# Performance work log

Measured on AMD Instinct MI355X. Metric: run time of the kernel, lower is better.

## Reference

```python
import jax, jax.numpy as jnp
import numpy as np

N_NODES = 100000
N_EDGES = 1600000
IN_FEATS = 64
N_CLASSES = 64


def setup_inputs() -> dict:
    key = jax.random.key(0)
    k1, k2, k3, k4, k5 = jax.random.split(key, 5)
    feat = jax.random.normal(k1, (N_NODES, IN_FEATS), dtype=jnp.float32)
    edge_row = jnp.sort(jax.random.randint(k2, (N_EDGES,), 0, N_NODES))
    edge_col = jax.random.randint(k3, (N_EDGES,), 0, N_NODES)
    # values of the cached normalized adjacency power (all positive, ~1/deg scale)
    edge_val = jax.random.uniform(k4, (N_EDGES,), dtype=jnp.float32) / 16.0
    # nn.Linear(in_feats, n_classes): weight [C, F] (xavier), bias zeros
    limit = float(np.sqrt(6.0 / (IN_FEATS + N_CLASSES)))
    W = jax.random.uniform(k5, (N_CLASSES, IN_FEATS), dtype=jnp.float32,
                           minval=-limit, maxval=limit)
    b = jnp.zeros((N_CLASSES,), dtype=jnp.float32)
    return {"feat": feat, "edge_row": edge_row, "edge_col": edge_col,
            "edge_val": edge_val, "W": W, "b": b}


def reference(feat, edge_row, edge_col, edge_val, W, b):
    # SpMM: h = A_pre @ feat, A_pre given as COO (edge_row, edge_col, edge_val)
    msg = edge_val[:, None] * feat[edge_col]          # [E, F] gather + scale
    h = jax.ops.segment_sum(msg, edge_row, num_segments=N_NODES)  # [N, F]
    # fc: Linear(in_feats -> n_classes), norm=None so no normalization
    return h @ W.T + b                                 # [N, C]
```

## Files before the change

kernel.cpp:

```cpp
#include <hip/hip_runtime.h>
#include <hip/hip_bf16.h>

typedef __attribute__((ext_vector_type(8))) short short8;
typedef __attribute__((ext_vector_type(4))) float f32x4;

__device__ __forceinline__ unsigned short f2bf(float x) {
    unsigned int u = __float_as_uint(x);
    unsigned int lsb = (u >> 16) & 1u;
    u += 0x7fffu + lsb;
    return (unsigned short)(u >> 16);
}

__device__ __forceinline__ float bf2f(unsigned short b) {
    return __uint_as_float(((unsigned int)b) << 16);
}

__device__ __forceinline__ short8 pack8(float4 a, float4 b) {
    short8 r;
    r[0] = (short)f2bf(a.x); r[1] = (short)f2bf(a.y);
    r[2] = (short)f2bf(a.z); r[3] = (short)f2bf(a.w);
    r[4] = (short)f2bf(b.x); r[5] = (short)f2bf(b.y);
    r[6] = (short)f2bf(b.z); r[7] = (short)f2bf(b.w);
    return r;
}

__global__ __launch_bounds__(256) void k_init(const float* __restrict__ bias,
                                              float* __restrict__ out, long total4) {
    long i4 = (long)blockIdx.x * 256 + threadIdx.x;
    if (i4 < total4) {
        const float4* b4 = (const float4*)bias;
        ((float4*)out)[i4] = b4[i4 & 15];
    }
}

__global__ __launch_bounds__(256) void k_setup(const float* __restrict__ feat,
                                               const float* __restrict__ W,
                                               const float* __restrict__ bias,
                                               unsigned short* __restrict__ G,
                                               float* __restrict__ out,
                                               int N, int gblocks) {
    if ((int)blockIdx.x >= gblocks) {
        long i4 = (long)(blockIdx.x - gblocks) * 256 + threadIdx.x;
        long total4 = (long)N * 16;
        if (i4 < total4) {
            const float4* b4 = (const float4*)bias;
            ((float4*)out)[i4] = b4[i4 & 15];
        }
        return;
    }

    int wave = blockIdx.x * 4 + (threadIdx.x >> 6);
    int lane = threadIdx.x & 63;
    int m0 = wave * 16;
    if (m0 >= N) return;
    int n = lane & 15;
    int quad = lane >> 4;

    short8 bf[4][2];
#pragma unroll
    for (int ct = 0; ct < 4; ++ct)
#pragma unroll
        for (int ks = 0; ks < 2; ++ks) {
            const float* wp = W + (size_t)(ct * 16 + n) * 64 + ks * 32 + quad * 8;
            float4 w0 = *(const float4*)wp;
            float4 w1 = *(const float4*)(wp + 4);
            bf[ct][ks] = pack8(w0, w1);
        }

    int mrow = m0 + n; if (mrow >= N) mrow = N - 1;
    short8 af[2];
#pragma unroll
    for (int ks = 0; ks < 2; ++ks) {
        const float* ap = feat + (size_t)mrow * 64 + ks * 32 + quad * 8;
        float4 a0 = *(const float4*)ap;
        float4 a1 = *(const float4*)(ap + 4);
        af[ks] = pack8(a0, a1);
    }

    f32x4 acc[4];
#pragma unroll
    for (int ct = 0; ct < 4; ++ct) {
        acc[ct] = (f32x4){0.f, 0.f, 0.f, 0.f};
#pragma unroll
        for (int ks = 0; ks < 2; ++ks)
            acc[ct] = __builtin_amdgcn_mfma_f32_16x16x32_bf16(af[ks], bf[ct][ks], acc[ct], 0, 0, 0);
    }

#pragma unroll
    for (int ct = 0; ct < 4; ++ct)
#pragma unroll
        for (int r = 0; r < 4; ++r) {
            int rowm = m0 + quad * 4 + r;
            if (rowm < N)
                G[(size_t)rowm * 64 + ct * 16 + n] = f2bf(acc[ct][r]);
        }
}

__global__ __launch_bounds__(256) void k_spmm(const unsigned short* __restrict__ G,
                                              const int* __restrict__ erow,
                                              const int* __restrict__ ecol,
                                              const float* __restrict__ evalv,
                                              float* __restrict__ out,
                                              int E, int cpw) {
    int wave = blockIdx.x * 4 + (threadIdx.x >> 6);
    int lane = threadIdx.x & 63;
    long base0 = (long)wave * cpw * 64;
    if (base0 >= E) return;

    int cur = __builtin_amdgcn_readfirstlane(erow[base0]);
    float acc = 0.f;

    for (int ch = 0; ch < cpw; ++ch) {
        long base = base0 + (long)ch * 64;
        if (base >= E) break;
        long idx = base + lane;
        long cidx = idx < E ? idx : (long)(E - 1);
        int rv = erow[cidx];
        int cv = ecol[cidx];
        float vvf = (idx < E) ? evalv[cidx] : 0.f;
        int vv = __float_as_int(vvf);

#pragma unroll
        for (int j0 = 0; j0 < 64; j0 += 16) {
            float g[16];
#pragma unroll
            for (int u = 0; u < 16; ++u) {
                int c = __builtin_amdgcn_readlane(cv, j0 + u);
                g[u] = bf2f(G[((size_t)(unsigned)c << 6) | (unsigned)lane]);
            }
#pragma unroll
            for (int u = 0; u < 16; ++u) {
                int r = __builtin_amdgcn_readlane(rv, j0 + u);
                float v = __int_as_float(__builtin_amdgcn_readlane(vv, j0 + u));
                if (r != cur) {
                    atomicAdd(out + ((size_t)(unsigned)cur << 6) + lane, acc);
                    acc = 0.f;
                    cur = r;
                }
                acc = fmaf(v, g[u], acc);
            }
        }
    }
    atomicAdd(out + ((size_t)(unsigned)cur << 6) + lane, acc);
}

__global__ __launch_bounds__(256) void k_fused(const float* __restrict__ feat,
                                               const int* __restrict__ erow,
                                               const int* __restrict__ ecol,
                                               const float* __restrict__ evalv,
                                               const float* __restrict__ W,
                                               float* __restrict__ out,
                                               int E, int epw) {
    __shared__ float Wt[64 * 64];
    for (int i = threadIdx.x; i < 4096; i += 256) {
        int c = i >> 6, f = i & 63;
        Wt[f * 64 + c] = W[i];
    }
    __syncthreads();

    int wave = blockIdx.x * 4 + (threadIdx.x >> 6);
    int lane = threadIdx.x & 63;
    long e0 = (long)wave * epw;
    if (e0 >= E) return;
    long e1 = e0 + epw; if (e1 > E) e1 = E;

    int cur = erow[e0];
    float acc = 0.f;
    for (long e = e0; e < e1; ++e) {
        int r = erow[e];
        int c = ecol[e];
        float v = evalv[e];
        float g = feat[((size_t)c << 6) | lane];
        if (r != cur) {
            float res = 0.f;
#pragma unroll
            for (int f = 0; f < 64; ++f)
                res += __shfl(acc, f, 64) * Wt[f * 64 + lane];
            atomicAdd(out + ((size_t)cur << 6) + lane, res);
            acc = 0.f;
            cur = r;
        }
        acc += v * g;
    }
    {
        float res = 0.f;
#pragma unroll
        for (int f = 0; f < 64; ++f)
            res += __shfl(acc, f, 64) * Wt[f * 64 + lane];
        atomicAdd(out + ((size_t)cur << 6) + lane, res);
    }
}

extern "C" void kernel_launch(void* const* d_in, const int* in_sizes, int n_in,
                              void* d_out, int out_size, void* d_ws, size_t ws_size,
                              hipStream_t stream) {
    const float* feat  = (const float*)d_in[0];
    const int*   erow  = (const int*)d_in[1];
    const int*   ecol  = (const int*)d_in[2];
    const float* evalv = (const float*)d_in[3];
    const float* W     = (const float*)d_in[4];
    const float* bias  = (const float*)d_in[5];
    float* out = (float*)d_out;

    int N = in_sizes[0] / 64;
    int E = in_sizes[1];

    size_t need = (size_t)N * 64 * sizeof(unsigned short);
    if (ws_size >= need) {
        unsigned short* G = (unsigned short*)d_ws;
        int tiles = (N + 15) / 16;
        int gblocks = (tiles + 3) / 4;
        long total4 = (long)N * 16;
        int iblocks = (int)((total4 + 255) / 256);
        k_setup<<<gblocks + iblocks, 256, 0, stream>>>(feat, W, bias, G, out, N, gblocks);

        const int cpw = 4;
        int nchunks = (E + 63) / 64;
        int nwaves = (nchunks + cpw - 1) / cpw;
        int nblocks = (nwaves + 3) / 4;
        k_spmm<<<nblocks, 256, 0, stream>>>(G, erow, ecol, evalv, out, E, cpw);
    } else {
        long total4 = (long)N * 16;
        k_init<<<(int)((total4 + 255) / 256), 256, 0, stream>>>(bias, out, total4);
        int epw = (E + 8191) / 8192;
        if (epw < 32) epw = 32;
        int nwaves = (E + epw - 1) / epw;
        int nblocks = (nwaves + 3) / 4;
        k_fused<<<nblocks, 256, 0, stream>>>(feat, erow, ecol, evalv, W, out, E, epw);
    }
}
```

Measured before the change: 141.8 us.

## Process two edges per wave step with 32-bit bf16-pair gathers in SpMM

The SpMM wave now splits into two half-waves that each handle a different edge. Each lane gathers a packed pair of bf16 values as one 32-bit load, so a single load instruction covers two edges' feature rows. This is meant to halve the number of gather instructions and readlane-driven loop iterations per edge. Row flushes now combine the two halves with a cross-lane shuffle before the atomics, and the per-pair branch adds divergence logic. Nontemporal loads and stores are added for the streaming edge arrays, feat and the bias init, and chunks per wave drop from 4 to 2 to give more parallel waves.

```diff
diff --git a/kernel.cpp b/kernel.cpp
--- a/kernel.cpp
+++ b/kernel.cpp
@@ -11,11 +11,11 @@
     return (unsigned short)(u >> 16);
 }
 
-__device__ __forceinline__ float bf2f(unsigned short b) {
-    return __uint_as_float(((unsigned int)b) << 16);
-}
-
-__device__ __forceinline__ short8 pack8(float4 a, float4 b) {
+__device__ __forceinline__ float bf2f(unsigned int b16) {
+    return __uint_as_float(b16 << 16);
+}
+
+__device__ __forceinline__ short8 pack8(f32x4 a, f32x4 b) {
     short8 r;
     r[0] = (short)f2bf(a.x); r[1] = (short)f2bf(a.y);
     r[2] = (short)f2bf(a.z); r[3] = (short)f2bf(a.w);
@@ -28,8 +28,8 @@
                                               float* __restrict__ out, long total4) {
     long i4 = (long)blockIdx.x * 256 + threadIdx.x;
     if (i4 < total4) {
-        const float4* b4 = (const float4*)bias;
-        ((float4*)out)[i4] = b4[i4 & 15];
+        const f32x4* b4 = (const f32x4*)bias;
+        ((f32x4*)out)[i4] = b4[i4 & 15];
     }
 }
 
@@ -43,8 +43,9 @@
         long i4 = (long)(blockIdx.x - gblocks) * 256 + threadIdx.x;
         long total4 = (long)N * 16;
         if (i4 < total4) {
-            const float4* b4 = (const float4*)bias;
-            ((float4*)out)[i4] = b4[i4 & 15];
+            const f32x4* b4 = (const f32x4*)bias;
+            f32x4 v = b4[i4 & 15];
+            __builtin_nontemporal_store(v, (f32x4*)out + i4);
         }
         return;
     }
@@ -61,9 +62,9 @@
     for (int ct = 0; ct < 4; ++ct)
 #pragma unroll
         for (int ks = 0; ks < 2; ++ks) {
-            const float* wp = W + (size_t)(ct * 16 + n) * 64 + ks * 32 + quad * 8;
-            float4 w0 = *(const float4*)wp;
-            float4 w1 = *(const float4*)(wp + 4);
+            const f32x4* wp = (const f32x4*)(W + (size_t)(ct * 16 + n) * 64 + ks * 32 + quad * 8);
+            f32x4 w0 = wp[0];
+            f32x4 w1 = wp[1];
             bf[ct][ks] = pack8(w0, w1);
         }
 
@@ -71,9 +72,9 @@
     short8 af[2];
 #pragma unroll
     for (int ks = 0; ks < 2; ++ks) {
-        const float* ap = feat + (size_t)mrow * 64 + ks * 32 + quad * 8;
-        float4 a0 = *(const float4*)ap;
-        float4 a1 = *(const float4*)(ap + 4);
+        const f32x4* ap = (const f32x4*)(feat + (size_t)mrow * 64 + ks * 32 + quad * 8);
+        f32x4 a0 = __builtin_nontemporal_load(ap);
+        f32x4 a1 = __builtin_nontemporal_load(ap + 1);
         af[ks] = pack8(a0, a1);
     }
 
@@ -96,7 +97,18 @@
         }
 }
 
-__global__ __launch_bounds__(256) void k_spmm(const unsigned short* __restrict__ G,
+__device__ __forceinline__ void flush_row(float* __restrict__ out, int row,
+                                          int s, int h, float a0, float a1) {
+    a0 += __shfl_xor(a0, 32, 64);
+    a1 += __shfl_xor(a1, 32, 64);
+    if (h == 0) {
+        float* p = out + ((size_t)(unsigned)row << 6) + (s << 1);
+        atomicAdd(p, a0);
+        atomicAdd(p + 1, a1);
+    }
+}
+
+__global__ __launch_bounds__(256) void k_spmm(const unsigned* __restrict__ Gd,
                                               const int* __restrict__ erow,
                                               const int* __restrict__ ecol,
                                               const float* __restrict__ evalv,
@@ -104,44 +116,68 @@
                                               int E, int cpw) {
     int wave = blockIdx.x * 4 + (threadIdx.x >> 6);
     int lane = threadIdx.x & 63;
+    int h = lane >> 5;
+    int s = lane & 31;
     long base0 = (long)wave * cpw * 64;
     if (base0 >= E) return;
 
     int cur = __builtin_amdgcn_readfirstlane(erow[base0]);
-    float acc = 0.f;
+    float acc0 = 0.f, acc1 = 0.f;
 
     for (int ch = 0; ch < cpw; ++ch) {
         long base = base0 + (long)ch * 64;
         if (base >= E) break;
         long idx = base + lane;
         long cidx = idx < E ? idx : (long)(E - 1);
-        int rv = erow[cidx];
-        int cv = ecol[cidx];
-        float vvf = (idx < E) ? evalv[cidx] : 0.f;
-        int vv = __float_as_int(vvf);
-
-#pragma unroll
-        for (int j0 = 0; j0 < 64; j0 += 16) {
-            float g[16];
+        int rv = __builtin_nontemporal_load(erow + cidx);
+        int cv = __builtin_nontemporal_load(ecol + cidx);
+        float vf = (idx < E) ? __builtin_nontemporal_load(evalv + cidx) : 0.f;
+        int vv = __float_as_int(vf);
+
+#pragma unroll
+        for (int j0 = 0; j0 < 32; j0 += 16) {
+            unsigned g[16];
 #pragma unroll
             for (int u = 0; u < 16; ++u) {
-                int c = __builtin_amdgcn_readlane(cv, j0 + u);
-                g[u] = bf2f(G[((size_t)(unsigned)c << 6) | (unsigned)lane]);
+                int p = j0 + u;
+                int c0 = __builtin_amdgcn_readlane(cv, 2 * p);
+                int c1 = __builtin_amdgcn_readlane(cv, 2 * p + 1);
+                int cc = h ? c1 : c0;
+                g[u] = Gd[(size_t)(unsigned)cc * 32u + (unsigned)s];
             }
 #pragma unroll
             for (int u = 0; u < 16; ++u) {
-                int r = __builtin_amdgcn_readlane(rv, j0 + u);
-                float v = __int_as_float(__builtin_amdgcn_readlane(vv, j0 + u));
-                if (r != cur) {
-                    atomicAdd(out + ((size_t)(unsigned)cur << 6) + lane, acc);
-                    acc = 0.f;
-                    cur = r;
+                int p = j0 + u;
+                int r0 = __builtin_amdgcn_readlane(rv, 2 * p);
+                int r1 = __builtin_amdgcn_readlane(rv, 2 * p + 1);
+                float v0 = __int_as_float(__builtin_amdgcn_readlane(vv, 2 * p));
+                float v1 = __int_as_float(__builtin_amdgcn_readlane(vv, 2 * p + 1));
+                float g0 = bf2f(g[u] & 0xffffu);
+                float g1 = bf2f(g[u] >> 16);
+                if (r0 == cur && r1 == cur) {
+                    float vh = h ? v1 : v0;
+                    acc0 = fmaf(vh, g0, acc0);
+                    acc1 = fmaf(vh, g1, acc1);
+                } else {
+                    if (r0 != cur) {
+                        flush_row(out, cur, s, h, acc0, acc1);
+                        acc0 = 0.f; acc1 = 0.f; cur = r0;
+                    }
+                    float ve0 = (h == 0) ? v0 : 0.f;
+                    acc0 = fmaf(ve0, g0, acc0);
+                    acc1 = fmaf(ve0, g1, acc1);
+                    if (r1 != cur) {
+                        flush_row(out, cur, s, h, acc0, acc1);
+                        acc0 = 0.f; acc1 = 0.f; cur = r1;
+                    }
+                    float ve1 = (h == 1) ? v1 : 0.f;
+                    acc0 = fmaf(ve1, g0, acc0);
+                    acc1 = fmaf(ve1, g1, acc1);
                 }
-                acc = fmaf(v, g[u], acc);
             }
         }
     }
-    atomicAdd(out + ((size_t)(unsigned)cur << 6) + lane, acc);
+    flush_row(out, cur, s, h, acc0, acc1);
 }
 
 __global__ __launch_bounds__(256) void k_fused(const float* __restrict__ feat,
@@ -214,11 +250,11 @@
         int iblocks = (int)((total4 + 255) / 256);
         k_setup<<<gblocks + iblocks, 256, 0, stream>>>(feat, W, bias, G, out, N, gblocks);
 
-        const int cpw = 4;
+        const int cpw = 2;
         int nchunks = (E + 63) / 64;
         int nwaves = (nchunks + cpw - 1) / cpw;
         int nblocks = (nwaves + 3) / 4;
-        k_spmm<<<nblocks, 256, 0, stream>>>(G, erow, ecol, evalv, out, E, cpw);
+        k_spmm<<<nblocks, 256, 0, stream>>>((const unsigned*)G, erow, ecol, evalv, out, E, cpw);
     } else {
         long total4 = (long)N * 16;
         k_init<<<(int)((total4 + 255) / 256), 256, 0, stream>>>(bias, out, total4);
```

After: 164.1 us. 1.16x slower.
